# Optimization experiments

Hardware: AMD Instinct MI355X
Metric: run time of the kernel (lower is better)

The kernel has to match this reference:

```python
import jax, jax.numpy as jnp
import numpy as np

NUM_HEADS = 8
HEAD_DIM = 128
MAX_RES = 224.0


def rope_embed(feat_shape, dim, max_res=MAX_RES):
    # timm pixel_freq_bands: 2**linspace(0, log2(max_res)-1, dim//4) * pi
    num_bands = dim // 4
    bands = (2.0 ** jnp.linspace(0.0, float(np.log2(max_res)) - 1.0, num_bands)) * jnp.pi
    # pixel coords in [-1, 1] per spatial dim
    coords = [jnp.linspace(-1.0, 1.0, s) for s in feat_shape]
    grid = jnp.stack(jnp.meshgrid(*coords, indexing='ij'), axis=-1)[..., None]  # [H,W,2,1]
    pos = grid * bands  # [H,W,2,num_bands]
    n = int(np.prod(feat_shape))
    sin = jnp.repeat(jnp.sin(pos).reshape(n, -1), 2, axis=-1)  # [n, dim]
    cos = jnp.repeat(jnp.cos(pos).reshape(n, -1), 2, axis=-1)  # [n, dim]
    return sin, cos


def _rot(x):
    # interleaved rotate-half: (x0,x1,x2,x3,...) -> (-x1,x0,-x3,x2,...)
    return jnp.stack([-x[..., 1::2], x[..., ::2]], axis=-1).reshape(x.shape)


def setup_inputs() -> dict:
    key = jax.random.key(0)
    k1, k2, k3, k4 = jax.random.split(key, 4)
    C, E = 1024, 1024
    x = jax.random.normal(k1, (64, C, 16, 16), dtype=jnp.float32)
    qkv_w = jax.random.normal(k2, (3 * E, C), dtype=jnp.float32) * (C ** -0.5)
    qkv_b = jnp.zeros((3 * E,), dtype=jnp.float32)
    proj_w = jax.random.normal(k3, (E, E), dtype=jnp.float32) * (E ** -0.5)
    proj_b = jax.random.normal(k4, (E,), dtype=jnp.float32) * 0.02
    return {"x": x, "qkv_w": qkv_w, "qkv_b": qkv_b, "proj_w": proj_w, "proj_b": proj_b}


def reference(x, qkv_w, qkv_b, proj_w, proj_b):
    B, C, H, W = x.shape
    n = H * W
    scale = HEAD_DIM ** -0.5
    sin_emb, cos_emb = rope_embed((H, W), HEAD_DIM)  # [n, head_dim]

    t = x.reshape(B, C, n).transpose(0, 2, 1)                      # [B, n, C]
    t = jnp.concatenate([t.mean(axis=1, keepdims=True), t], axis=1)  # [B, n+1, C]

    qkv = t @ qkv_w.T + qkv_b                                      # [B, n+1, 3E]
    qkv = qkv.reshape(B, n + 1, 3, NUM_HEADS, HEAD_DIM).transpose(2, 0, 3, 1, 4)
    q, k, v = qkv[0], qkv[1], qkv[2]                               # [B, h, n+1, d]

    def apply_rope(z):
        zc, zs = z[:, :, :1], z[:, :, 1:]
        zs = zs * cos_emb + _rot(zs) * sin_emb
        return jnp.concatenate([zc, zs], axis=2)

    q = apply_rope(q)
    k = apply_rope(k)

    attn = jax.nn.softmax(jnp.einsum('bhqd,bhkd->bhqk', q, k) * scale, axis=-1)
    out = jnp.einsum('bhqk,bhkd->bhqd', attn, v)
    out = out.transpose(0, 2, 1, 3).reshape(B, n + 1, -1)           # [B, n+1, E]
    out = out @ proj_w.T + proj_b
    return out[:, 0]
```

## Files before the change

kernel.cpp:

```cpp
#include <hip/hip_runtime.h>
#include <math.h>

#define PI_F 3.14159265358979323846f
#define KSTEP 0.21959209425992272f

using bf16x8 = __attribute__((ext_vector_type(8))) short;
using f32x4 = __attribute__((ext_vector_type(4))) float;
using u16x8 = __attribute__((ext_vector_type(8))) unsigned short;

static __device__ __forceinline__ float wave_reduce_sum(float v) {
#pragma unroll
  for (int off = 32; off; off >>= 1) v += __shfl_down(v, off);
  return v;
}

static __device__ __forceinline__ unsigned short f2bf(float f) {
  unsigned u = __float_as_uint(f);
  return (unsigned short)((u + 0x7fffu + ((u >> 16) & 1u)) >> 16);
}

static __device__ __forceinline__ void gload_lds16(const void* g, void* l) {
  __builtin_amdgcn_global_load_lds((const __attribute__((address_space(1))) unsigned int*)g,
                                   (__attribute__((address_space(3))) unsigned int*)l, 16, 0, 0);
}

__global__ __launch_bounds__(256) void prep_kernel(const float* __restrict__ x,
                                                   const float* __restrict__ qkv_w,
                                                   unsigned short* __restrict__ xt,
                                                   float* __restrict__ t_mean,
                                                   unsigned short* __restrict__ wk_bf,
                                                   float2* __restrict__ sc) {
  const int bid = blockIdx.x;
  const int t = threadIdx.x;
  __shared__ float tile[64][33];
  if (bid < 1024) {
    const int ct = bid & 15, b = bid >> 4;
    const int cl = t >> 2, pq = (t & 3) * 8;
    const int pl = t >> 3, cq = (t & 7) * 8;
    float sum = 0.0f;
    const float* xrow = x + ((size_t)(b * 1024 + ct * 64 + cl) * 256) + pq;
    unsigned short* xtb = xt + (size_t)b * 262144 + ct * 64;
    for (int pt = 0; pt < 8; ++pt) {
      const float4 v0 = *reinterpret_cast<const float4*>(xrow + pt * 32);
      const float4 v1 = *reinterpret_cast<const float4*>(xrow + pt * 32 + 4);
      tile[cl][pq + 0] = v0.x; tile[cl][pq + 1] = v0.y; tile[cl][pq + 2] = v0.z; tile[cl][pq + 3] = v0.w;
      tile[cl][pq + 4] = v1.x; tile[cl][pq + 5] = v1.y; tile[cl][pq + 6] = v1.z; tile[cl][pq + 7] = v1.w;
      sum += (v0.x + v0.y) + (v0.z + v0.w) + (v1.x + v1.y) + (v1.z + v1.w);
      __syncthreads();
      u16x8 o;
#pragma unroll
      for (int e = 0; e < 8; ++e) o[e] = f2bf(tile[cq + e][pl]);
      *reinterpret_cast<u16x8*>(xtb + (size_t)(pt * 32 + pl) * 1024 + cq) = o;
      __syncthreads();
    }
    sum += __shfl_xor(sum, 1);
    sum += __shfl_xor(sum, 2);
    if ((t & 3) == 0) t_mean[b * 1024 + ct * 64 + cl] = sum * (1.0f / 256.0f);
  } else if (bid < 2048) {
    const int i = ((bid - 1024) * 256 + t) * 4;
    const float4 v = *reinterpret_cast<const float4*>(qkv_w + 1048576 + i);
    ushort4 r;
    r.x = f2bf(v.x); r.y = f2bf(v.y); r.z = f2bf(v.z); r.w = f2bf(v.w);
    *reinterpret_cast<ushort4*>(wk_bf + i) = r;
  } else {
    const int idx = (bid - 2048) * 256 + t;
    const int m = idx >> 8, j = idx & 255;
    const float band = exp2f((float)(m & 31) * KSTEP) * PI_F;
    const float coord = (m < 32) ? (-1.0f + (2.0f / 15.0f) * (float)(j >> 4))
                                 : (-1.0f + (2.0f / 15.0f) * (float)(j & 15));
    float sn, cs;
    sincosf(coord * band, &sn, &cs);
    sc[idx] = make_float2(sn, cs);
  }
}

__global__ __launch_bounds__(256) void gemm_splitk(
    const float* __restrict__ A, int lda, int aStrideZ,
    const float* __restrict__ B, int ldb, int bStrideZ,
    float* __restrict__ Cp, int ldc, int cStrideZ, int cStrideKc, int KC) {
  const int nt = blockIdx.x, mt = blockIdx.y;
  const int z = blockIdx.z / KC, kc = blockIdx.z % KC;
  const int tid = threadIdx.x;
  A += (size_t)z * aStrideZ + (size_t)mt * 32 * lda + kc * 256;
  B += (size_t)z * bStrideZ + (size_t)nt * 64 * ldb + kc * 256;
  Cp += (size_t)kc * cStrideKc + (size_t)z * cStrideZ + (size_t)mt * 32 * ldc + nt * 64;

  __shared__ float As[32][34];
  __shared__ float Bs[32][68];

  const int tm = tid >> 4;
  const int tn = tid & 15;
  float acc0[4] = {0, 0, 0, 0}, acc1[4] = {0, 0, 0, 0};

  for (int k0 = 0; k0 < 256; k0 += 32) {
    {
      const int m = tid >> 3, kq = tid & 7;
      float4 v = *reinterpret_cast<const float4*>(A + (size_t)m * lda + k0 + kq * 4);
      As[kq * 4 + 0][m] = v.x; As[kq * 4 + 1][m] = v.y;
      As[kq * 4 + 2][m] = v.z; As[kq * 4 + 3][m] = v.w;
    }
#pragma unroll
    for (int r = 0; r < 2; ++r) {
      const int idx = r * 256 + tid;
      const int n = idx >> 3, kq = idx & 7;
      float4 v = *reinterpret_cast<const float4*>(B + (size_t)n * ldb + k0 + kq * 4);
      Bs[kq * 4 + 0][n] = v.x; Bs[kq * 4 + 1][n] = v.y;
      Bs[kq * 4 + 2][n] = v.z; Bs[kq * 4 + 3][n] = v.w;
    }
    __syncthreads();
#pragma unroll
    for (int k = 0; k < 32; ++k) {
      const float a0 = As[k][tm * 2], a1 = As[k][tm * 2 + 1];
      const float4 bb = *reinterpret_cast<const float4*>(&Bs[k][tn * 4]);
      acc0[0] += a0 * bb.x; acc0[1] += a0 * bb.y; acc0[2] += a0 * bb.z; acc0[3] += a0 * bb.w;
      acc1[0] += a1 * bb.x; acc1[1] += a1 * bb.y; acc1[2] += a1 * bb.z; acc1[3] += a1 * bb.w;
    }
    __syncthreads();
  }
  *reinterpret_cast<float4*>(Cp + (size_t)(tm * 2) * ldc + tn * 4) =
      make_float4(acc0[0], acc0[1], acc0[2], acc0[3]);
  *reinterpret_cast<float4*>(Cp + (size_t)(tm * 2 + 1) * ldc + tn * 4) =
      make_float4(acc1[0], acc1[1], acc1[2], acc1[3]);
}

__global__ __launch_bounds__(256) void reduce4_bias(const float* __restrict__ part,
                                                    const float* __restrict__ bias,
                                                    float* __restrict__ out) {
  const int i = blockIdx.x * 256 + threadIdx.x;
  out[i] = part[i] + part[i + 65536] + part[i + 131072] + part[i + 196608] + bias[i & 1023];
}

__global__ __launch_bounds__(512) void k_scores_mfma(
    const unsigned short* __restrict__ wk, const unsigned short* __restrict__ xt,
    const float* __restrict__ qkv_b, const float* __restrict__ q0p,
    const float2* __restrict__ sc, float* __restrict__ S) {
  const int l = blockIdx.x;
  const int b = (l & 7) + ((l >> 6) << 3);
  const int h = (l >> 3) & 7;
  const int tid = threadIdx.x;
  const int w = tid >> 6, lane = tid & 63;
  const int wm = (w >> 2) * 64, wn = (w & 3) * 64;

  __shared__ __align__(16) char smem[49152];
  char* As = smem;
  char* Bs = smem + 16384;

  const int rowA = lane >> 3, ci = lane & 7;
  const unsigned short* wkh = wk + (size_t)h * 128 * 1024;
  const unsigned short* xtb = xt + (size_t)b * 262144;

  f32x4 acc[4][4] = {};

  for (int kt = 0; kt < 16; ++kt) {
    const int c0 = kt * 64;
#pragma unroll
    for (int i = 0; i < 2; ++i) {
      const int d = (w * 2 + i) * 8 + rowA;
      gload_lds16(wkh + (size_t)d * 1024 + c0 + ((ci ^ (d & 7)) * 8), As + (w * 2 + i) * 1024);
    }
#pragma unroll
    for (int i = 0; i < 4; ++i) {
      const int j = (w * 4 + i) * 8 + rowA;
      gload_lds16(xtb + (size_t)j * 1024 + c0 + ((ci ^ (j & 7)) * 8), Bs + (w * 4 + i) * 1024);
    }
    __syncthreads();
#pragma unroll
    for (int kk = 0; kk < 2; ++kk) {
      const int coff = kk * 64 + (lane >> 4) * 16;
      bf16x8 af[4], bfr[4];
#pragma unroll
      for (int mi = 0; mi < 4; ++mi) {
        const int d = wm + mi * 16 + (lane & 15);
        af[mi] = *reinterpret_cast<const bf16x8*>(As + d * 128 + (coff ^ ((d & 7) << 4)));
      }
#pragma unroll
      for (int ni = 0; ni < 4; ++ni) {
        const int j = wn + ni * 16 + (lane & 15);
        bfr[ni] = *reinterpret_cast<const bf16x8*>(Bs + j * 128 + (coff ^ ((j & 7) << 4)));
      }
#pragma unroll
      for (int mi = 0; mi < 4; ++mi)
#pragma unroll
        for (int ni = 0; ni < 4; ++ni)
          acc[mi][ni] = __builtin_amdgcn_mfma_f32_16x16x32_bf16(af[mi], bfr[ni], acc[mi][ni], 0, 0, 0);
    }
    __syncthreads();
  }

  float* q0_lds = reinterpret_cast<float*>(smem + 40960);
  if (tid < 128) {
    const float* qp = q0p + (size_t)b * 2048 + h * 128 + tid;
    q0_lds[tid] = qkv_b[h * 128 + tid] + qp[0] + qp[131072] + qp[262144] + qp[393216];
  }
  __syncthreads();

  const float* bk = qkv_b + 1024 + h * 128;
  const int colj = lane & 15, rgrp = lane >> 4;
  float partial[4] = {0, 0, 0, 0};
#pragma unroll
  for (int mi = 0; mi < 4; ++mi) {
#pragma unroll
    for (int pp = 0; pp < 2; ++pp) {
      const int d0 = wm + mi * 16 + rgrp * 4 + pp * 2;
      const int m = d0 >> 1;
      const float2 qv = *reinterpret_cast<const float2*>(q0_lds + d0);
      const float2 bv = *reinterpret_cast<const float2*>(bk + d0);
#pragma unroll
      for (int ni = 0; ni < 4; ++ni) {
        const int j = wn + ni * 16 + colj;
        const float ke = acc[mi][ni][pp * 2] + bv.x;
        const float ko = acc[mi][ni][pp * 2 + 1] + bv.y;
        const float2 t = sc[m * 256 + j];
        const float P = ke * qv.x + ko * qv.y;
        const float Q = ke * qv.y - ko * qv.x;
        partial[ni] += t.y * P + t.x * Q;
      }
    }
  }
  float* red = reinterpret_cast<float*>(smem);
#pragma unroll
  for (int ni = 0; ni < 4; ++ni)
    red[(wn + ni * 16 + colj) * 9 + (w >> 2) * 4 + rgrp] = partial[ni];
  __syncthreads();
  if (tid < 256) {
    float s = 0.0f;
#pragma unroll
    for (int k = 0; k < 8; ++k) s += red[tid * 9 + k];
    S[(size_t)(b * 8 + h) * 257 + 1 + tid] = s;
  }
}

__global__ __launch_bounds__(64) void softmax_kernel(const float* __restrict__ q0p,
                                                     const float* __restrict__ qkv_b,
                                                     const float* __restrict__ S,
                                                     float* __restrict__ attn) {
  const int bh = blockIdx.x;
  const int b = bh >> 3, h = bh & 7;
  const int l = threadIdx.x;
  const float scale = 0.08838834764831845f;
  float q0a = qkv_b[h * 128 + l], q0b = qkv_b[h * 128 + l + 64];
  float k0a = qkv_b[1024 + h * 128 + l], k0b = qkv_b[1024 + h * 128 + l + 64];
  const float* base = q0p + (size_t)b * 2048;
#pragma unroll
  for (int kc = 0; kc < 4; ++kc) {
    const float* pp = base + (size_t)kc * 131072;
    q0a += pp[h * 128 + l];
    q0b += pp[h * 128 + l + 64];
    k0a += pp[1024 + h * 128 + l];
    k0b += pp[1024 + h * 128 + l + 64];
  }
  float p = q0a * k0a + q0b * k0b;
  p = wave_reduce_sum(p);
  const float s0 = __shfl(p, 0);
  const float* Sb = S + (size_t)bh * 257;
  float v[5];
  float mx = -3.0e38f;
  int cnt = 0;
  for (int j = l; j < 257; j += 64) {
    const float s = ((j == 0) ? s0 : Sb[j]) * scale;
    v[cnt++] = s;
    mx = fmaxf(mx, s);
  }
#pragma unroll
  for (int off = 32; off; off >>= 1) mx = fmaxf(mx, __shfl_xor(mx, off));
  float sum = 0.0f;
  for (int i = 0; i < cnt; ++i) {
    v[i] = expf(v[i] - mx);
    sum += v[i];
  }
#pragma unroll
  for (int off = 32; off; off >>= 1) sum += __shfl_xor(sum, off);
  const float inv = 1.0f / sum;
  int i = 0;
  for (int j = l; j < 257; j += 64) attn[(size_t)bh * 257 + j] = v[i++] * inv;
}

__global__ __launch_bounds__(256) void u_accum_kernel(const float* __restrict__ x,
                                                      const float* __restrict__ t_mean,
                                                      const float* __restrict__ attn,
                                                      float* __restrict__ u) {
  const int ct = blockIdx.x;
  const int b = blockIdx.y;
  const int tid = threadIdx.x;
  __shared__ float aw[257 * 8];
  __shared__ float red[2048];
  for (int i = tid; i < 257 * 8; i += 256) {
    const int j = i >> 3, h = i & 7;
    aw[i] = attn[(size_t)(b * 8 + h) * 257 + j];
  }
  __syncthreads();
  const int cl = tid >> 2, q = tid & 3;
  const int c = ct * 64 + cl;
  const float* xr = x + ((size_t)b * 1024 + c) * 256 + q * 64;
  float acc[8] = {};
#pragma unroll 4
  for (int p4 = 0; p4 < 64; p4 += 4) {
    const float4 xv = *reinterpret_cast<const float4*>(xr + p4);
    const int pbase = q * 64 + p4 + 1;
    const float xs[4] = {xv.x, xv.y, xv.z, xv.w};
#pragma unroll
    for (int e = 0; e < 4; ++e) {
      const float* w8 = &aw[(pbase + e) * 8];
#pragma unroll
      for (int h = 0; h < 8; ++h) acc[h] += w8[h] * xs[e];
    }
  }
  if (q == 0) {
    const float tm = t_mean[b * 1024 + c];
#pragma unroll
    for (int h = 0; h < 8; ++h) acc[h] += aw[h] * tm;
  }
#pragma unroll
  for (int h = 0; h < 8; ++h) red[(cl * 4 + q) * 8 + h] = acc[h];
  __syncthreads();
#pragma unroll
  for (int r = 0; r < 2; ++r) {
    const int o = tid * 2 + r;
    const int cl2 = o >> 3, h = o & 7;
    const float s = red[(cl2 * 4 + 0) * 8 + h] + red[(cl2 * 4 + 1) * 8 + h] +
                    red[(cl2 * 4 + 2) * 8 + h] + red[(cl2 * 4 + 3) * 8 + h];
    u[(size_t)(b * 8 + h) * 1024 + ct * 64 + cl2] = s;
  }
}

extern "C" void kernel_launch(void* const* d_in, const int* in_sizes, int n_in,
                              void* d_out, int out_size, void* d_ws, size_t ws_size,
                              hipStream_t stream) {
  const float* x = (const float*)d_in[0];
  const float* qkv_w = (const float*)d_in[1];
  const float* qkv_b = (const float*)d_in[2];
  const float* proj_w = (const float*)d_in[3];
  const float* proj_b = (const float*)d_in[4];
  float* out = (float*)d_out;

  float* ws = (float*)d_ws;
  float* t_mean = ws;
  float* q0k0_part = ws + 65536;
  float* S = ws + 589824;
  float* attn = ws + 721408;
  float* u = ws + 852992;
  float* out0 = ws + 1377280;
  float* out0_part = ws + 1442816;
  float* out_part = ws + 1704960;
  float2* sc = (float2*)(ws + 1967104);
  unsigned short* wk_bf = (unsigned short*)(ws + 1999872);
  unsigned short* x_t = (unsigned short*)(ws + 2524160);

  prep_kernel<<<2112, 256, 0, stream>>>(x, qkv_w, x_t, t_mean, wk_bf, sc);

  gemm_splitk<<<dim3(32, 2, 4), 256, 0, stream>>>(t_mean, 1024, 0, qkv_w, 1024, 0,
                                                  q0k0_part, 2048, 0, 131072, 4);

  k_scores_mfma<<<512, 512, 0, stream>>>(wk_bf, x_t, qkv_b, q0k0_part, sc, S);

  softmax_kernel<<<512, 64, 0, stream>>>(q0k0_part, qkv_b, S, attn);

  u_accum_kernel<<<dim3(16, 64), 256, 0, stream>>>(x, t_mean, attn, u);

  gemm_splitk<<<dim3(2, 2, 32), 256, 0, stream>>>(u, 8192, 1024,
                                                  qkv_w + (size_t)2048 * 1024, 1024, 131072,
                                                  out0_part, 1024, 128, 65536, 4);
  reduce4_bias<<<256, 256, 0, stream>>>(out0_part, qkv_b + 2048, out0);

  gemm_splitk<<<dim3(16, 2, 4), 256, 0, stream>>>(out0, 1024, 0, proj_w, 1024, 0,
                                                  out_part, 1024, 0, 65536, 4);
  reduce4_bias<<<256, 256, 0, stream>>>(out_part, proj_b, out);
}
```

Baseline: 114.7 us.

## Double-buffer score GEMM, read bf16 transposed x in u_accum, fuse reduce into proj GEMM

The key-score MFMA kernel is split across two column tiles, which doubles the grid, and it now double-buffers its LDS loads so the next K slice is fetched while the current one computes. u_accum now reads the bf16 transposed x with coalesced row loads instead of fp32 x, which halves the bytes read but adds bf16 rounding to the value path. The split-K reduction plus bias of the V-projection output is folded into the A-tile load of a new projection GEMM, removing one launch and an intermediate buffer.

After: 114.0 us. Within noise of the previous version (-0.6%).

```diff
diff --git a/kernel.cpp b/kernel.cpp
--- a/kernel.cpp
+++ b/kernel.cpp
@@ -17,6 +17,10 @@
 static __device__ __forceinline__ unsigned short f2bf(float f) {
   unsigned u = __float_as_uint(f);
   return (unsigned short)((u + 0x7fffu + ((u >> 16) & 1u)) >> 16);
+}
+
+static __device__ __forceinline__ float bf2f(unsigned short s) {
+  return __uint_as_float(((unsigned)s) << 16);
 }
 
 static __device__ __forceinline__ void gload_lds16(const void* g, void* l) {
@@ -123,6 +127,59 @@
       make_float4(acc1[0], acc1[1], acc1[2], acc1[3]);
 }
 
+__global__ __launch_bounds__(256) void gemm_proj_splitk(
+    const float* __restrict__ Apart, const float* __restrict__ abias,
+    const float* __restrict__ B, float* __restrict__ Cp) {
+  const int nt = blockIdx.x, mt = blockIdx.y, kc = blockIdx.z;
+  const int tid = threadIdx.x;
+  B += (size_t)nt * 64 * 1024 + kc * 256;
+  Cp += (size_t)kc * 65536 + (size_t)mt * 32 * 1024 + nt * 64;
+
+  __shared__ float As[32][34];
+  __shared__ float Bs[32][68];
+
+  const int tm = tid >> 4;
+  const int tn = tid & 15;
+  float acc0[4] = {0, 0, 0, 0}, acc1[4] = {0, 0, 0, 0};
+
+  for (int k0 = 0; k0 < 256; k0 += 32) {
+    {
+      const int m = tid >> 3, kq = tid & 7;
+      const int kg = kc * 256 + k0 + kq * 4;
+      const float* Ab = Apart + (size_t)(mt * 32 + m) * 1024 + kg;
+      float4 v = *reinterpret_cast<const float4*>(abias + kg);
+#pragma unroll
+      for (int r = 0; r < 4; ++r) {
+        const float4 p = *reinterpret_cast<const float4*>(Ab + (size_t)r * 65536);
+        v.x += p.x; v.y += p.y; v.z += p.z; v.w += p.w;
+      }
+      As[kq * 4 + 0][m] = v.x; As[kq * 4 + 1][m] = v.y;
+      As[kq * 4 + 2][m] = v.z; As[kq * 4 + 3][m] = v.w;
+    }
+#pragma unroll
+    for (int r = 0; r < 2; ++r) {
+      const int idx = r * 256 + tid;
+      const int n = idx >> 3, kq = idx & 7;
+      float4 v = *reinterpret_cast<const float4*>(B + (size_t)n * 1024 + k0 + kq * 4);
+      Bs[kq * 4 + 0][n] = v.x; Bs[kq * 4 + 1][n] = v.y;
+      Bs[kq * 4 + 2][n] = v.z; Bs[kq * 4 + 3][n] = v.w;
+    }
+    __syncthreads();
+#pragma unroll
+    for (int k = 0; k < 32; ++k) {
+      const float a0 = As[k][tm * 2], a1 = As[k][tm * 2 + 1];
+      const float4 bb = *reinterpret_cast<const float4*>(&Bs[k][tn * 4]);
+      acc0[0] += a0 * bb.x; acc0[1] += a0 * bb.y; acc0[2] += a0 * bb.z; acc0[3] += a0 * bb.w;
+      acc1[0] += a1 * bb.x; acc1[1] += a1 * bb.y; acc1[2] += a1 * bb.z; acc1[3] += a1 * bb.w;
+    }
+    __syncthreads();
+  }
+  *reinterpret_cast<float4*>(Cp + (size_t)(tm * 2) * 1024 + tn * 4) =
+      make_float4(acc0[0], acc0[1], acc0[2], acc0[3]);
+  *reinterpret_cast<float4*>(Cp + (size_t)(tm * 2 + 1) * 1024 + tn * 4) =
+      make_float4(acc1[0], acc1[1], acc1[2], acc1[3]);
+}
+
 __global__ __launch_bounds__(256) void reduce4_bias(const float* __restrict__ part,
                                                     const float* __restrict__ bias,
                                                     float* __restrict__ out) {
@@ -135,59 +192,67 @@
     const float* __restrict__ qkv_b, const float* __restrict__ q0p,
     const float2* __restrict__ sc, float* __restrict__ S) {
   const int l = blockIdx.x;
-  const int b = (l & 7) + ((l >> 6) << 3);
-  const int h = (l >> 3) & 7;
+  const int b = ((l >> 7) << 3) + (l & 7);
+  const int h = (l >> 4) & 7;
+  const int jt = (l >> 3) & 1;
   const int tid = threadIdx.x;
   const int w = tid >> 6, lane = tid & 63;
-  const int wm = (w >> 2) * 64, wn = (w & 3) * 64;
-
-  __shared__ __align__(16) char smem[49152];
-  char* As = smem;
-  char* Bs = smem + 16384;
+  const int wm = (w >> 2) * 64, wn = (w & 3) * 32;
+
+  __shared__ __align__(16) char smem[65536];
 
   const int rowA = lane >> 3, ci = lane & 7;
   const unsigned short* wkh = wk + (size_t)h * 128 * 1024;
-  const unsigned short* xtb = xt + (size_t)b * 262144;
-
-  f32x4 acc[4][4] = {};
-
+  const unsigned short* xtb = xt + (size_t)b * 262144 + (size_t)jt * 128 * 1024;
+
+  f32x4 acc[4][2] = {};
+
+#define STAGE(sel, c0)                                                                   \
+  {                                                                                      \
+    char* Ab = smem + (sel)*32768;                                                       \
+    char* Bb = Ab + 16384;                                                               \
+    _Pragma("unroll") for (int i = 0; i < 2; ++i) {                                      \
+      const int r = (w * 2 + i) * 8 + rowA;                                              \
+      gload_lds16(wkh + (size_t)r * 1024 + (c0) + ((ci ^ (r & 7)) * 8),                  \
+                  Ab + (w * 2 + i) * 1024);                                              \
+      gload_lds16(xtb + (size_t)r * 1024 + (c0) + ((ci ^ (r & 7)) * 8),                  \
+                  Bb + (w * 2 + i) * 1024);                                              \
+    }                                                                                    \
+  }
+
+  STAGE(0, 0);
+  __syncthreads();
+  int cur = 0;
   for (int kt = 0; kt < 16; ++kt) {
-    const int c0 = kt * 64;
-#pragma unroll
-    for (int i = 0; i < 2; ++i) {
-      const int d = (w * 2 + i) * 8 + rowA;
-      gload_lds16(wkh + (size_t)d * 1024 + c0 + ((ci ^ (d & 7)) * 8), As + (w * 2 + i) * 1024);
-    }
-#pragma unroll
-    for (int i = 0; i < 4; ++i) {
-      const int j = (w * 4 + i) * 8 + rowA;
-      gload_lds16(xtb + (size_t)j * 1024 + c0 + ((ci ^ (j & 7)) * 8), Bs + (w * 4 + i) * 1024);
-    }
-    __syncthreads();
+    if (kt < 15) STAGE(cur ^ 1, (kt + 1) * 64);
+    const char* Ab = smem + cur * 32768;
+    const char* Bb = Ab + 16384;
 #pragma unroll
     for (int kk = 0; kk < 2; ++kk) {
       const int coff = kk * 64 + (lane >> 4) * 16;
-      bf16x8 af[4], bfr[4];
+      bf16x8 af[4], bfr[2];
 #pragma unroll
       for (int mi = 0; mi < 4; ++mi) {
         const int d = wm + mi * 16 + (lane & 15);
-        af[mi] = *reinterpret_cast<const bf16x8*>(As + d * 128 + (coff ^ ((d & 7) << 4)));
+        af[mi] = *reinterpret_cast<const bf16x8*>(Ab + d * 128 + (coff ^ ((d & 7) << 4)));
       }
 #pragma unroll
-      for (int ni = 0; ni < 4; ++ni) {
+      for (int ni = 0; ni < 2; ++ni) {
         const int j = wn + ni * 16 + (lane & 15);
-        bfr[ni] = *reinterpret_cast<const bf16x8*>(Bs + j * 128 + (coff ^ ((j & 7) << 4)));
+        bfr[ni] = *reinterpret_cast<const bf16x8*>(Bb + j * 128 + (coff ^ ((j & 7) << 4)));
       }
 #pragma unroll
       for (int mi = 0; mi < 4; ++mi)
 #pragma unroll
-        for (int ni = 0; ni < 4; ++ni)
+        for (int ni = 0; ni < 2; ++ni)
           acc[mi][ni] = __builtin_amdgcn_mfma_f32_16x16x32_bf16(af[mi], bfr[ni], acc[mi][ni], 0, 0, 0);
     }
     __syncthreads();
-  }
-
-  float* q0_lds = reinterpret_cast<float*>(smem + 40960);
+    cur ^= 1;
+  }
+#undef STAGE
+
+  float* q0_lds = reinterpret_cast<float*>(smem + 57344);
   if (tid < 128) {
     const float* qp = q0p + (size_t)b * 2048 + h * 128 + tid;
     q0_lds[tid] = qkv_b[h * 128 + tid] + qp[0] + qp[131072] + qp[262144] + qp[393216];
@@ -196,7 +261,7 @@
 
   const float* bk = qkv_b + 1024 + h * 128;
   const int colj = lane & 15, rgrp = lane >> 4;
-  float partial[4] = {0, 0, 0, 0};
+  float partial[2] = {0, 0};
 #pragma unroll
   for (int mi = 0; mi < 4; ++mi) {
 #pragma unroll
@@ -206,8 +271,8 @@
       const float2 qv = *reinterpret_cast<const float2*>(q0_lds + d0);
       const float2 bv = *reinterpret_cast<const float2*>(bk + d0);
 #pragma unroll
-      for (int ni = 0; ni < 4; ++ni) {
-        const int j = wn + ni * 16 + colj;
+      for (int ni = 0; ni < 2; ++ni) {
+        const int j = jt * 128 + wn + ni * 16 + colj;
         const float ke = acc[mi][ni][pp * 2] + bv.x;
         const float ko = acc[mi][ni][pp * 2 + 1] + bv.y;
         const float2 t = sc[m * 256 + j];
@@ -219,14 +284,14 @@
   }
   float* red = reinterpret_cast<float*>(smem);
 #pragma unroll
-  for (int ni = 0; ni < 4; ++ni)
+  for (int ni = 0; ni < 2; ++ni)
     red[(wn + ni * 16 + colj) * 9 + (w >> 2) * 4 + rgrp] = partial[ni];
   __syncthreads();
-  if (tid < 256) {
+  if (tid < 128) {
     float s = 0.0f;
 #pragma unroll
     for (int k = 0; k < 8; ++k) s += red[tid * 9 + k];
-    S[(size_t)(b * 8 + h) * 257 + 1 + tid] = s;
+    S[(size_t)(b * 8 + h) * 257 + 1 + jt * 128 + tid] = s;
   }
 }
 
@@ -275,51 +340,45 @@
   for (int j = l; j < 257; j += 64) attn[(size_t)bh * 257 + j] = v[i++] * inv;
 }
 
-__global__ __launch_bounds__(256) void u_accum_kernel(const float* __restrict__ x,
+__global__ __launch_bounds__(256) void u_accum_kernel(const unsigned short* __restrict__ xt,
                                                       const float* __restrict__ t_mean,
                                                       const float* __restrict__ attn,
                                                       float* __restrict__ u) {
   const int ct = blockIdx.x;
   const int b = blockIdx.y;
   const int tid = threadIdx.x;
-  __shared__ float aw[257 * 8];
-  __shared__ float red[2048];
-  for (int i = tid; i < 257 * 8; i += 256) {
-    const int j = i >> 3, h = i & 7;
-    aw[i] = attn[(size_t)(b * 8 + h) * 257 + j];
-  }
+  __shared__ float aw[2056];
+  __shared__ float red[8192];
+  for (int i = tid; i < 2056; i += 256) aw[i] = attn[(size_t)(b * 8 + (i & 7)) * 257 + (i >> 3)];
   __syncthreads();
-  const int cl = tid >> 2, q = tid & 3;
-  const int c = ct * 64 + cl;
-  const float* xr = x + ((size_t)b * 1024 + c) * 256 + q * 64;
-  float acc[8] = {};
-#pragma unroll 4
-  for (int p4 = 0; p4 < 64; p4 += 4) {
-    const float4 xv = *reinterpret_cast<const float4*>(xr + p4);
-    const int pbase = q * 64 + p4 + 1;
-    const float xs[4] = {xv.x, xv.y, xv.z, xv.w};
-#pragma unroll
-    for (int e = 0; e < 4; ++e) {
-      const float* w8 = &aw[(pbase + e) * 8];
-#pragma unroll
-      for (int h = 0; h < 8; ++h) acc[h] += w8[h] * xs[e];
-    }
-  }
-  if (q == 0) {
-    const float tm = t_mean[b * 1024 + c];
-#pragma unroll
-    for (int h = 0; h < 8; ++h) acc[h] += aw[h] * tm;
-  }
-#pragma unroll
-  for (int h = 0; h < 8; ++h) red[(cl * 4 + q) * 8 + h] = acc[h];
+  const int cl = tid & 31, q = tid >> 5;
+  const int c = ct * 128 + cl * 4;
+  const unsigned short* xr = xt + (size_t)b * 262144 + c;
+  float acc[8][4] = {};
+  for (int p = q * 32; p < q * 32 + 32; ++p) {
+    const ushort4 v = *reinterpret_cast<const ushort4*>(xr + (size_t)p * 1024);
+    const float xs[4] = {bf2f(v.x), bf2f(v.y), bf2f(v.z), bf2f(v.w)};
+    const float* w8 = &aw[(p + 1) * 8];
+#pragma unroll
+    for (int hh = 0; hh < 8; ++hh)
+#pragma unroll
+      for (int e = 0; e < 4; ++e) acc[hh][e] += w8[hh] * xs[e];
+  }
+#pragma unroll
+  for (int hh = 0; hh < 8; ++hh)
+#pragma unroll
+    for (int e = 0; e < 4; ++e) red[q * 1024 + (cl * 8 + hh) * 4 + e] = acc[hh][e];
   __syncthreads();
 #pragma unroll
-  for (int r = 0; r < 2; ++r) {
-    const int o = tid * 2 + r;
-    const int cl2 = o >> 3, h = o & 7;
-    const float s = red[(cl2 * 4 + 0) * 8 + h] + red[(cl2 * 4 + 1) * 8 + h] +
-                    red[(cl2 * 4 + 2) * 8 + h] + red[(cl2 * 4 + 3) * 8 + h];
-    u[(size_t)(b * 8 + h) * 1024 + ct * 64 + cl2] = s;
+  for (int r = 0; r < 4; ++r) {
+    const int o = tid * 4 + r;
+    const int cl2 = o >> 5, hh = (o >> 2) & 7, e = o & 3;
+    float s = 0.0f;
+#pragma unroll
+    for (int qq = 0; qq < 8; ++qq) s += red[qq * 1024 + o];
+    const int cc = ct * 128 + cl2 * 4 + e;
+    s += aw[hh] * t_mean[b * 1024 + cc];
+    u[(size_t)(b * 8 + hh) * 1024 + cc] = s;
   }
 }
 
@@ -339,30 +398,28 @@
   float* S = ws + 589824;
   float* attn = ws + 721408;
   float* u = ws + 852992;
-  float* out0 = ws + 1377280;
-  float* out0_part = ws + 1442816;
-  float* out_part = ws + 1704960;
-  float2* sc = (float2*)(ws + 1967104);
-  unsigned short* wk_bf = (unsigned short*)(ws + 1999872);
-  unsigned short* x_t = (unsigned short*)(ws + 2524160);
+  float* out0_part = ws + 1377280;
+  float* out_part = ws + 1639424;
+  float2* sc = (float2*)(ws + 1901568);
+  unsigned short* wk_bf = (unsigned short*)(ws + 1934336);
+  unsigned short* x_t = (unsigned short*)(ws + 2458624);
 
   prep_kernel<<<2112, 256, 0, stream>>>(x, qkv_w, x_t, t_mean, wk_bf, sc);
 
   gemm_splitk<<<dim3(32, 2, 4), 256, 0, stream>>>(t_mean, 1024, 0, qkv_w, 1024, 0,
                                                   q0k0_part, 2048, 0, 131072, 4);
 
-  k_scores_mfma<<<512, 512, 0, stream>>>(wk_bf, x_t, qkv_b, q0k0_part, sc, S);
+  k_scores_mfma<<<1024, 512, 0, stream>>>(wk_bf, x_t, qkv_b, q0k0_part, sc, S);
 
   softmax_kernel<<<512, 64, 0, stream>>>(q0k0_part, qkv_b, S, attn);
 
-  u_accum_kernel<<<dim3(16, 64), 256, 0, stream>>>(x, t_mean, attn, u);
+  u_accum_kernel<<<dim3(8, 64), 256, 0, stream>>>(x_t, t_mean, attn, u);
 
   gemm_splitk<<<dim3(2, 2, 32), 256, 0, stream>>>(u, 8192, 1024,
                                                   qkv_w + (size_t)2048 * 1024, 1024, 131072,
                                                   out0_part, 1024, 128, 65536, 4);
-  reduce4_bias<<<256, 256, 0, stream>>>(out0_part, qkv_b + 2048, out0);
-
-  gemm_splitk<<<dim3(16, 2, 4), 256, 0, stream>>>(out0, 1024, 0, proj_w, 1024, 0,
-                                                  out_part, 1024, 0, 65536, 4);
+
+  gemm_proj_splitk<<<dim3(16, 2, 4), 256, 0, stream>>>(out0_part, qkv_b + 2048, proj_w, out_part);
+
   reduce4_bias<<<256, 256, 0, stream>>>(out_part, proj_b, out);
 }
```
